# Kernel optimization log

Measured on AMD Instinct MI355X. Metric: run time of the kernel, lower is better.

## Reference

```python
import math
import jax, jax.numpy as jnp
import numpy as np

H = 1024        # hidden_size
V = 32000       # target vocab
T = 64          # decoder steps
B = 32          # batch
NL = 2          # lstm layers
WSZ = 50        # window_size
WLEN = 2 * WSZ + 1
L = 128         # source length (all sequences full)
S = L + WLEN    # padded encoder length, guarantees windows in-bounds
HH = math.ceil(H / 2)
STD2 = (WSZ / 2.0) ** 2
EPS = 1e-14


def setup_inputs():
    key = jax.random.key(0)
    ks = jax.random.split(key, 16)
    sc = 0.02
    inp = {}
    inp["encoder_output"] = jax.random.normal(ks[0], (S, B, H), jnp.float32)
    inp["context"] = jax.random.normal(ks[1], (T, B, H), jnp.float32)
    inp["h0"] = jax.random.normal(ks[2], (NL, B, H), jnp.float32)
    inp["c0"] = jax.random.normal(ks[3], (NL, B, H), jnp.float32)
    inp["embedding"] = jax.random.normal(ks[4], (V, H), jnp.float32) * sc
    inp["attn_w1"] = jax.random.normal(ks[5], (HH, H), jnp.float32) * sc
    inp["attn_b1"] = jnp.zeros((HH,), jnp.float32)
    inp["attn_w2"] = jax.random.normal(ks[6], (1, HH), jnp.float32) * sc
    inp["attn_b2"] = jnp.zeros((1,), jnp.float32)
    inp["lstm_Wih0"] = jax.random.normal(ks[7], (4 * H, 2 * H), jnp.float32) * sc  # input feeding: 2H input
    inp["lstm_Whh0"] = jax.random.normal(ks[8], (4 * H, H), jnp.float32) * sc
    inp["lstm_bih0"] = jnp.zeros((4 * H,), jnp.float32)
    inp["lstm_bhh0"] = jnp.zeros((4 * H,), jnp.float32)
    inp["lstm_Wih1"] = jax.random.normal(ks[9], (4 * H, H), jnp.float32) * sc
    inp["lstm_Whh1"] = jax.random.normal(ks[10], (4 * H, H), jnp.float32) * sc
    inp["lstm_bih1"] = jnp.zeros((4 * H,), jnp.float32)
    inp["lstm_bhh1"] = jnp.zeros((4 * H,), jnp.float32)
    inp["fc1_w"] = jax.random.normal(ks[11], (H, 2 * H), jnp.float32) * sc
    inp["fc1_b"] = jnp.zeros((H,), jnp.float32)
    inp["fc2_w"] = jax.random.normal(ks[12], (V, H), jnp.float32) * sc
    inp["fc2_b"] = jnp.zeros((V,), jnp.float32)
    inp["target_words"] = jax.random.randint(ks[13], (T, B), 0, V)
    inp["lengths"] = jnp.full((B,), L, dtype=jnp.int32)
    return inp


def _lstm_layer(x, h0, c0, Wih, Whh, bih, bhh):
    bias = bih + bhh
    def step(carry, xt):
        h, c = carry
        gates = xt @ Wih.T + h @ Whh.T + bias   # [B, 4H], torch gate order i,f,g,o
        i, f, g, o = jnp.split(gates, 4, axis=-1)
        c = jax.nn.sigmoid(f) * c + jax.nn.sigmoid(i) * jnp.tanh(g)
        h = jax.nn.sigmoid(o) * jnp.tanh(c)
        return (h, c), h
    (hT, cT), ys = jax.lax.scan(step, (h0, c0), x)
    return ys, hT, cT


def _attention(encoder_output, dec_out, lengths, aw1, ab1, aw2, ab2):
    h_s = jnp.transpose(encoder_output, (1, 0, 2))   # [B, S, H]
    h_t = jnp.transpose(dec_out, (1, 0, 2))          # [B, T, H]
    p = jax.nn.sigmoid(jnp.tanh(h_t @ aw1.T + ab1) @ aw2.T + ab2)[..., 0]  # [B, T]
    p = WSZ + lengths[:, None].astype(jnp.float32) * p
    win_start = jnp.round(p - WSZ).astype(jnp.int32)                        # [B, T]
    k = jnp.arange(WLEN)
    positions = win_start[..., None].astype(jnp.float32) + k.astype(jnp.float32)  # [B, T, W]
    gaussian = jnp.exp(-((positions - p[..., None]) ** 2) / (2.0 * STD2))
    # faithful to original: the selection buffer is overwritten every j, so
    # every decoder step attends over the LAST step's window
    sel_idx = win_start[:, -1][:, None] + k                                 # [B, W]
    selection = jnp.take_along_axis(h_s, sel_idx[:, :, None], axis=1)       # [B, W, H]
    score = jnp.einsum('bth,bwh->btw', h_t, selection)
    li = lengths[:, None, None].astype(jnp.int32)
    lo = k[None, None, :] < (WSZ - win_start)[..., None]
    hi = k[None, None, :] >= (li + WSZ - win_start[..., None])
    score = jnp.where(lo | hi, EPS, score)   # original writes epsilon, NOT -inf
    a = jax.nn.softmax(score, axis=2) * gaussian
    c = jnp.einsum('btw,bwh->bth', a, selection)
    return jnp.transpose(c, (1, 0, 2))       # [T, B, H]


def reference(encoder_output, context, h0, c0, embedding,
              attn_w1, attn_b1, attn_w2, attn_b2,
              lstm_Wih0, lstm_Whh0, lstm_bih0, lstm_bhh0,
              lstm_Wih1, lstm_Whh1, lstm_bih1, lstm_bhh1,
              fc1_w, fc1_b, fc2_w, fc2_b,
              target_words, lengths):
    emb = embedding[target_words]                        # [T, B, H]
    x = jnp.concatenate([emb, context], axis=2)          # input feeding -> [T, B, 2H]
    y0, hT0, cT0 = _lstm_layer(x, h0[0], c0[0], lstm_Wih0, lstm_Whh0, lstm_bih0, lstm_bhh0)
    y1, hT1, cT1 = _lstm_layer(y0, h0[1], c0[1], lstm_Wih1, lstm_Whh1, lstm_bih1, lstm_bhh1)
    ctx = _attention(encoder_output, y1, lengths, attn_w1, attn_b1, attn_w2, attn_b2)
    out = jax.nn.relu(jnp.concatenate([ctx, y1], axis=2) @ fc1_w.T + fc1_b)
    y = out @ fc2_w.T + fc2_b                            # [T, B, V]
    h_n = jnp.stack([hT0, hT1])
    c_n = jnp.stack([cT0, cT1])
    return (y, h_n, c_n, ctx)
```

## Files before the change

### kernel.cpp

```cpp
#include <hip/hip_runtime.h>
#include <hip/hip_bf16.h>

#define T_STEPS 64
#define BATCH   32
#define HID     1024
#define VOCAB   32000
#define WLEN_   101
#define WSZ_    50
#define SENC    229
#define LBLK    64

static const size_t Y_SZ   = (size_t)T_STEPS * BATCH * VOCAB;
static const size_t HN_SZ  = (size_t)2 * BATCH * HID;
static const size_t CTX_OFF = Y_SZ + 2 * HN_SZ;

typedef __attribute__((ext_vector_type(8)))  unsigned short us8;
typedef __attribute__((ext_vector_type(8)))  __bf16 bf16x8;
typedef __attribute__((ext_vector_type(4)))  float f32x4;
typedef __attribute__((ext_vector_type(16))) float f32x16;

static __device__ inline unsigned short f2bf(float x) {
    __hip_bfloat16 b = __float2bfloat16(x);
    return __builtin_bit_cast(unsigned short, b);
}

#define GLD_US8_SC(dst, ptr) \
    asm volatile("global_load_dwordx4 %0, %1, off sc0 sc1" : "=v"(dst) : "v"(ptr) : "memory")
#define GLD_F32_SC(dst, ptr) \
    asm volatile("global_load_dword %0, %1, off sc0 sc1" : "=v"(dst) : "v"(ptr) : "memory")
#define GST_U16_SC(ptr, val) \
    asm volatile("global_store_short %0, %1, off sc0 sc1" :: "v"(ptr), "v"(val) : "memory")
#define GST_U32_SC(ptr, val) \
    asm volatile("global_store_dword %0, %1, off sc0 sc1" :: "v"(ptr), "v"(val) : "memory")
#define WAIT_VM0() asm volatile("s_waitcnt vmcnt(0)" ::: "memory")

__global__ __launch_bounds__(256) void gemm_bt(
    const float* __restrict__ A, const float* __restrict__ W,
    const float* __restrict__ b1, const float* __restrict__ b2,
    float* __restrict__ out, int M, int N, int K, int act)
{
    __shared__ __align__(16) float As[16 * 132];
    __shared__ __align__(16) float Ws[16 * 68];
    const int tid  = threadIdx.x;
    const int col0 = blockIdx.x * 64;
    const int row0 = blockIdx.y * 128;
    const int ty   = tid >> 4;
    const int tx   = tid & 15;

    float acc[8][4];
#pragma unroll
    for (int i = 0; i < 8; ++i)
#pragma unroll
        for (int j = 0; j < 4; ++j) acc[i][j] = 0.f;

    for (int k0 = 0; k0 < K; k0 += 16) {
#pragma unroll
        for (int li = 0; li < 2; ++li) {
            int f  = tid + li * 256;
            int r  = f >> 2;
            int kq = (f & 3) << 2;
            float4 v = *reinterpret_cast<const float4*>(A + (size_t)(row0 + r) * K + k0 + kq);
            As[(kq + 0) * 132 + r] = v.x;
            As[(kq + 1) * 132 + r] = v.y;
            As[(kq + 2) * 132 + r] = v.z;
            As[(kq + 3) * 132 + r] = v.w;
        }
        {
            int n  = tid >> 2;
            int kq = (tid & 3) << 2;
            float4 v = *reinterpret_cast<const float4*>(W + (size_t)(col0 + n) * K + k0 + kq);
            Ws[(kq + 0) * 68 + n] = v.x;
            Ws[(kq + 1) * 68 + n] = v.y;
            Ws[(kq + 2) * 68 + n] = v.z;
            Ws[(kq + 3) * 68 + n] = v.w;
        }
        __syncthreads();
#pragma unroll
        for (int k = 0; k < 16; ++k) {
            const float4 a0 = *reinterpret_cast<const float4*>(&As[k * 132 + ty * 8]);
            const float4 a1 = *reinterpret_cast<const float4*>(&As[k * 132 + ty * 8 + 4]);
            const float4 b0 = *reinterpret_cast<const float4*>(&Ws[k * 68 + tx * 4]);
            float av[8] = {a0.x, a0.y, a0.z, a0.w, a1.x, a1.y, a1.z, a1.w};
            float bv[4] = {b0.x, b0.y, b0.z, b0.w};
#pragma unroll
            for (int i = 0; i < 8; ++i)
#pragma unroll
                for (int j = 0; j < 4; ++j) acc[i][j] = fmaf(av[i], bv[j], acc[i][j]);
        }
        __syncthreads();
    }

#pragma unroll
    for (int j = 0; j < 4; ++j) {
        int n = col0 + tx * 4 + j;
        float bias = 0.f;
        if (b1) bias += b1[n];
        if (b2) bias += b2[n];
#pragma unroll
        for (int i = 0; i < 8; ++i) {
            float v = acc[i][j] + bias;
            if (act == 1) v = fmaxf(v, 0.f);
            else if (act == 2) v = tanhf(v);
            out[(size_t)(row0 + ty * 8 + i) * N + n] = v;
        }
    }
}

__global__ __launch_bounds__(256) void gemm_lds_bt(
    const unsigned short* __restrict__ A, const unsigned short* __restrict__ W,
    const float* __restrict__ b1, const float* __restrict__ b2,
    float* __restrict__ out, unsigned short* __restrict__ out_bf,
    int M, int N, int K, int relu, int ntout)
{
    __shared__ __align__(16) unsigned short As[8192];
    __shared__ __align__(16) unsigned short Ws[8192];
    const int tid  = threadIdx.x;
    const int lane = tid & 63;
    const int wave = tid >> 6;

    const int nwg = gridDim.x;
    const int bid = blockIdx.x;
    const int q = nwg >> 3, r8 = nwg & 7;
    const int xcd = bid & 7, sidx = bid >> 3;
    const int wgid = (xcd < r8 ? xcd * (q + 1) : r8 * (q + 1) + (xcd - r8) * q) + sidx;
    const int mt = M >> 7;
    const int row0 = (wgid % mt) << 7;
    const int col0 = (wgid / mt) << 7;

    const int m0   = (wave >> 1) * 64;
    const int n0   = (wave & 1) * 64;
    const int lrow = lane & 15;
    const int kc   = lane >> 4;

    f32x4 acc[4][4];
#pragma unroll
    for (int i = 0; i < 4; ++i)
#pragma unroll
        for (int j = 0; j < 4; ++j) acc[i][j] = (f32x4){0.f, 0.f, 0.f, 0.f};

    const bool isA = (wave < 2);
    const int  lw  = wave & 1;
    const unsigned short* gbase = isA ? (A + (size_t)row0 * K) : (W + (size_t)col0 * K);
    unsigned short* lbase = isA ? As : Ws;

    for (int k0 = 0; k0 < K; k0 += 64) {
#pragma unroll
        for (int i = 0; i < 8; ++i) {
            const int c    = lw * 512 + i * 64 + lane;
            const int row  = c >> 3;
            const int slot = c & 7;
            const unsigned short* src =
                gbase + (size_t)row * K + k0 + ((slot ^ (row & 7)) << 3);
            __builtin_amdgcn_global_load_lds(
                (const __attribute__((address_space(1))) void*)src,
                (__attribute__((address_space(3))) void*)(lbase + (size_t)(lw * 512 + i * 64) * 8),
                16, 0, 0);
        }
        __syncthreads();
#pragma unroll
        for (int ss = 0; ss < 2; ++ss) {
            us8 a[4], b[4];
#pragma unroll
            for (int f = 0; f < 4; ++f) {
                const int ar = m0 + f * 16 + lrow;
                const int as = (ss * 4 + kc) ^ (ar & 7);
                a[f] = *reinterpret_cast<const us8*>(&As[(ar * 8 + as) * 8]);
                const int br = n0 + f * 16 + lrow;
                const int bs = (ss * 4 + kc) ^ (br & 7);
                b[f] = *reinterpret_cast<const us8*>(&Ws[(br * 8 + bs) * 8]);
            }
#pragma unroll
            for (int fi = 0; fi < 4; ++fi)
#pragma unroll
                for (int fj = 0; fj < 4; ++fj)
                    acc[fi][fj] = __builtin_amdgcn_mfma_f32_16x16x32_bf16(
                        __builtin_bit_cast(bf16x8, a[fi]),
                        __builtin_bit_cast(bf16x8, b[fj]),
                        acc[fi][fj], 0, 0, 0);
        }
        __syncthreads();
    }

#pragma unroll
    for (int fi = 0; fi < 4; ++fi)
#pragma unroll
        for (int fj = 0; fj < 4; ++fj) {
            const int cN = col0 + n0 + fj * 16 + lrow;
            float bv = 0.f;
            if (b1) bv += b1[cN];
            if (b2) bv += b2[cN];
#pragma unroll
            for (int j = 0; j < 4; ++j) {
                const int r = row0 + m0 + fi * 16 + (lane >> 4) * 4 + j;
                float v = acc[fi][fj][j] + bv;
                if (relu) v = fmaxf(v, 0.f);
                if (out) {
                    if (ntout) __builtin_nontemporal_store(v, &out[(size_t)r * N + cN]);
                    else       out[(size_t)r * N + cN] = v;
                }
                if (out_bf) out_bf[(size_t)r * N + cN] = f2bf(v);
            }
        }
}

__global__ void prep_kernel(const float* __restrict__ Wih0, unsigned short* __restrict__ Wih0_bf,
                            const float* __restrict__ fc1w, unsigned short* __restrict__ fc1w_bf,
                            const float* __restrict__ emb, const float* __restrict__ ctxin,
                            const int* __restrict__ tw, unsigned short* __restrict__ x_bf,
                            int* __restrict__ flags)
{
    const int bid = blockIdx.x, tid = threadIdx.x;
    if (bid < 2048) {
#pragma unroll
        for (int k = 0; k < 2; ++k) {
            int i = bid * 256 + tid + k * 524288;
            float4 v0 = *reinterpret_cast<const float4*>(Wih0 + (size_t)i * 8);
            float4 v1 = *reinterpret_cast<const float4*>(Wih0 + (size_t)i * 8 + 4);
            us8 c = {f2bf(v0.x), f2bf(v0.y), f2bf(v0.z), f2bf(v0.w),
                     f2bf(v1.x), f2bf(v1.y), f2bf(v1.z), f2bf(v1.w)};
            *reinterpret_cast<us8*>(Wih0_bf + (size_t)i * 8) = c;
        }
    } else if (bid < 3072) {
        int i = (bid - 2048) * 256 + tid;
        float4 v0 = *reinterpret_cast<const float4*>(fc1w + (size_t)i * 8);
        float4 v1 = *reinterpret_cast<const float4*>(fc1w + (size_t)i * 8 + 4);
        us8 c = {f2bf(v0.x), f2bf(v0.y), f2bf(v0.z), f2bf(v0.w),
                 f2bf(v1.x), f2bf(v1.y), f2bf(v1.z), f2bf(v1.w)};
        *reinterpret_cast<us8*>(fc1w_bf + (size_t)i * 8) = c;
    } else if (bid < 3584) {
#pragma unroll
        for (int k = 0; k < 4; ++k) {
            int idx = (bid - 3072) * 256 + tid + k * 131072;
            int row = idx >> 8;
            int c8  = idx & 255;
            const float* src = (c8 < 128)
                ? emb + (size_t)tw[row] * HID + c8 * 8
                : ctxin + (size_t)row * HID + (c8 - 128) * 8;
            float4 v0 = *reinterpret_cast<const float4*>(src);
            float4 v1 = *reinterpret_cast<const float4*>(src + 4);
            us8 c = {f2bf(v0.x), f2bf(v0.y), f2bf(v0.z), f2bf(v0.w),
                     f2bf(v1.x), f2bf(v1.y), f2bf(v1.z), f2bf(v1.w)};
            *reinterpret_cast<us8*>(x_bf + (size_t)idx * 8) = c;
        }
    } else {
        for (int i = tid; i < 6400; i += 256) flags[i] = 0;
    }
}

static __device__ inline void poll_group(int* __restrict__ flags, int gbase, int target)
{
    if (target <= 0) return;
    const int lane = threadIdx.x & 63;
    int* fp = &flags[(gbase + lane) * 32];
    for (;;) {
        int f = __hip_atomic_load(fp, __ATOMIC_RELAXED, __HIP_MEMORY_SCOPE_AGENT);
        if (__all(f >= target)) break;
        __builtin_amdgcn_s_sleep(1);
    }
}

__global__ __launch_bounds__(256) void lstm_fused3(
    const float* __restrict__ gpre0,
    const float* __restrict__ Whh0, const float* __restrict__ Wih1,
    const float* __restrict__ Whh1,
    const float* __restrict__ bih1, const float* __restrict__ bhh1,
    const float* __restrict__ h0all, const float* __restrict__ c0all,
    float* __restrict__ y1o,
    unsigned short* __restrict__ fin_bf,
    float* __restrict__ hn, float* __restrict__ cn,
    unsigned short* __restrict__ hbf,
    float* __restrict__ part,
    int* __restrict__ flags,
    const float* __restrict__ fc2w, unsigned short* __restrict__ fc2w_bf,
    int foldcvt)
{
    __shared__ __align__(16) us8 WB[8192];
    __shared__ float red2[32 * 132];
    __shared__ float csh[512];

    const int tid  = threadIdx.x;
    const int lane = tid & 63;
    const int w    = tid >> 6;
    const int n    = lane & 31;
    const int kh   = lane >> 5;
    const int bid  = blockIdx.x;
    const int role = bid >> 6;
    const int lb   = bid & 63;
    const int j0   = lb * 16;
    const int b    = tid >> 3;
    const int jj   = tid & 7;

    unsigned short* hb0 = hbf;
    unsigned short* hb1 = hbf + 131072;

    {
        const float* Wsrc = (role == 0) ? Whh0 : (role == 1 ? Wih1 : Whh1);
        const int g = n >> 3, cj = n & 7;
#pragma unroll
        for (int T = 0; T < 2; ++T) {
            const float* wrow = Wsrc + (size_t)(g * HID + j0 + T * 8 + cj) * HID;
#pragma unroll
            for (int f = 0; f < 16; ++f) {
                int k = w * 256 + f * 16 + kh * 8;
                float4 v0 = *reinterpret_cast<const float4*>(wrow + k);
                float4 v1 = *reinterpret_cast<const float4*>(wrow + k + 4);
                WB[((T * 4 + w) * 16 + f) * 64 + lane] =
                    (us8){f2bf(v0.x), f2bf(v0.y), f2bf(v0.z), f2bf(v0.w),
                          f2bf(v1.x), f2bf(v1.y), f2bf(v1.z), f2bf(v1.w)};
            }
        }
    }

    float gp[2][4] = {};
    float bb[2][4] = {};
    if (role == 0) {
#pragma unroll
        for (int T = 0; T < 2; ++T) {
            csh[T * 256 + tid] = c0all[b * HID + j0 + T * 8 + jj];
#pragma unroll
            for (int g = 0; g < 4; ++g)
                gp[T][g] = gpre0[(size_t)b * 4096 + g * HID + j0 + T * 8 + jj];
        }
#pragma unroll
        for (int q = 0; q < 2; ++q) {
            int e = lb * 512 + q * 256 + tid;
            unsigned int hv = f2bf(h0all[((e >> 3) & 31) * HID + (e >> 8) * 8 + (e & 7)]);
            GST_U16_SC(hb0 + e, hv);
        }
    } else if (role == 2) {
#pragma unroll
        for (int T = 0; T < 2; ++T) {
            csh[T * 256 + tid] = c0all[32768 + b * HID + j0 + T * 8 + jj];
#pragma unroll
            for (int g = 0; g < 4; ++g)
                bb[T][g] = bih1[g * HID + j0 + T * 8 + jj] + bhh1[g * HID + j0 + T * 8 + jj];
        }
#pragma unroll
        for (int q = 0; q < 2; ++q) {
            int e = lb * 512 + q * 256 + tid;
            unsigned int hv = f2bf(h0all[32768 + ((e >> 3) & 31) * HID + (e >> 8) * 8 + (e & 7)]);
            GST_U16_SC(hb1 + 32768 + e, hv);
        }
    }

    WAIT_VM0();
    __syncthreads();
    if (tid == 0)
        __hip_atomic_store(&flags[bid * 32], 1, __ATOMIC_RELAXED, __HIP_MEMORY_SCOPE_AGENT);

    for (int p = 0; p <= 65; ++p) {
        {
            int g1, t1, g2, t2;
            if (role == 0)      { g1 = 0;   t1 = p + 1; g2 = 64;  t2 = p - 1; }
            else if (role == 1) { g1 = 0;   t1 = p + 1; g2 = 128; t2 = p - 1; }
            else                { g1 = 64;  t1 = p + 1; g2 = 128; t2 = p + 1; }
            if (tid < 64)        poll_group(flags, g1, t1);
            else if (tid < 128)  poll_group(flags, g2, t2);
            __syncthreads();
        }
        const bool active = (role == 0) ? (p <= 63)
                          : (role == 1) ? (p >= 1 && p <= 64)
                                        : (p >= 2);
        if (active) {
            const int t = p - role;
            float pv[2][4];
            if (role == 2) {
                const float* pb = part + (size_t)((p - 2) & 3) * 131072 + lb * 2048 + tid;
#pragma unroll
                for (int T = 0; T < 2; ++T)
#pragma unroll
                    for (int g = 0; g < 4; ++g)
                        GLD_F32_SC(pv[T][g], pb + (T * 4 + g) * 256);
            }
            const unsigned short* hsrc = (role == 2)
                ? hb1 + ((p + 1) & 1) * 32768
                : hb0 + (p & 3) * 32768;
            const unsigned short* hr = hsrc + (size_t)w * 8192 + lane * 8;
            us8 aF[16];
#pragma unroll
            for (int f = 0; f < 16; ++f)
                GLD_US8_SC(aF[f], hr + f * 512);
            WAIT_VM0();
            __builtin_amdgcn_sched_barrier(0);

            f32x16 acc0 = {}, acc1 = {};
#pragma unroll
            for (int f = 0; f < 16; ++f)
                acc0 = __builtin_amdgcn_mfma_f32_32x32x16_bf16(
                    __builtin_bit_cast(bf16x8, aF[f]),
                    __builtin_bit_cast(bf16x8, WB[((0 * 4 + w) * 16 + f) * 64 + lane]),
                    acc0, 0, 0, 0);
#pragma unroll
            for (int f = 0; f < 16; ++f)
                acc1 = __builtin_amdgcn_mfma_f32_32x32x16_bf16(
                    __builtin_bit_cast(bf16x8, aF[f]),
                    __builtin_bit_cast(bf16x8, WB[((1 * 4 + w) * 16 + f) * 64 + lane]),
                    acc1, 0, 0, 0);

#pragma unroll
            for (int T = 0; T < 2; ++T) {
                if (T == 1) __syncthreads();
#pragma unroll
                for (int r = 0; r < 16; ++r) {
                    int m = (r & 3) + 8 * (r >> 2) + 4 * kh;
                    red2[m * 132 + w * 32 + n] = (T == 0) ? acc0[r] : acc1[r];
                }
                __syncthreads();
                float s0, s1, s2, s3;
                {
                    const float* rr = &red2[b * 132 + jj];
                    s0 = rr[0]  + rr[32]  + rr[64]  + rr[96];
                    s1 = rr[8]  + rr[40]  + rr[72]  + rr[104];
                    s2 = rr[16] + rr[48]  + rr[80]  + rr[112];
                    s3 = rr[24] + rr[56]  + rr[88]  + rr[120];
                }
                const int col = j0 + T * 8 + jj;
                const int he  = (lb * 2 + T) * 256 + tid;
                if (role == 1) {
                    float* pdst = part + (size_t)((p - 1) & 3) * 131072 + lb * 2048 + tid;
                    GST_U32_SC(pdst + (T * 4 + 0) * 256, s0);
                    GST_U32_SC(pdst + (T * 4 + 1) * 256, s1);
                    GST_U32_SC(pdst + (T * 4 + 2) * 256, s2);
                    GST_U32_SC(pdst + (T * 4 + 3) * 256, s3);
                } else {
                    if (role == 0) { s0 += gp[T][0]; s1 += gp[T][1]; s2 += gp[T][2]; s3 += gp[T][3]; }
                    else { s0 += pv[T][0] + bb[T][0]; s1 += pv[T][1] + bb[T][1];
                           s2 += pv[T][2] + bb[T][2]; s3 += pv[T][3] + bb[T][3]; }
                    float ig = 1.f / (1.f + expf(-s0));
                    float fg = 1.f / (1.f + expf(-s1));
                    float gg = tanhf(s2);
                    float og = 1.f / (1.f + expf(-s3));
                    float cv = fg * csh[T * 256 + tid] + ig * gg;
                    csh[T * 256 + tid] = cv;
                    float h = og * tanhf(cv);
                    unsigned int hv = f2bf(h);
                    if (role == 0) {
                        GST_U16_SC(hb0 + ((p + 1) & 3) * 32768 + he, hv);
                        if (t == T_STEPS - 1) { hn[b * HID + col] = h; cn[b * HID + col] = cv; }
                    } else {
                        __builtin_nontemporal_store(h, &y1o[(size_t)t * 32768 + b * HID + col]);
                        fin_bf[(size_t)(t * BATCH + b) * 2048 + 1024 + col] = f2bf(h);
                        if (t == T_STEPS - 1) {
                            hn[32768 + b * HID + col] = h;
                            cn[32768 + b * HID + col] = cv;
                        } else {
                            GST_U16_SC(hb1 + (p & 1) * 32768 + he, hv);
                        }
                    }
                }
            }
        }
        if (p < 65) {
            WAIT_VM0();
            __syncthreads();
            if (tid == 0)
                __hip_atomic_store(&flags[bid * 32], p + 2,
                                   __ATOMIC_RELAXED, __HIP_MEMORY_SCOPE_AGENT);
            if (role == 0 && p + 1 <= 63) {
                const float* gsrc = gpre0 + (size_t)((p + 1) * BATCH + b) * 4096 + j0 + jj;
#pragma unroll
                for (int T = 0; T < 2; ++T)
#pragma unroll
                    for (int g = 0; g < 4; ++g)
                        gp[T][g] = gsrc[g * HID + T * 8];
            }
            if (foldcvt && p < 64 && bid >= 64) {
                const int cidx = bid - 64;
                const int base = (p * 128 + cidx) * 500;
                for (int j = tid; j < 500; j += 256) {
                    int i = base + j;
                    if (i < 4096000) {
                        float4 v0 = *reinterpret_cast<const float4*>(fc2w + (size_t)i * 8);
                        float4 v1 = *reinterpret_cast<const float4*>(fc2w + (size_t)i * 8 + 4);
                        us8 c = {f2bf(v0.x), f2bf(v0.y), f2bf(v0.z), f2bf(v0.w),
                                 f2bf(v1.x), f2bf(v1.y), f2bf(v1.z), f2bf(v1.w)};
                        *reinterpret_cast<us8*>(fc2w_bf + (size_t)i * 8) = c;
                    }
                }
            }
        }
    }
}

__global__ __launch_bounds__(64) void attn_p_kernel(
    const float* __restrict__ hidden1, const float* __restrict__ aw2,
    const float* __restrict__ ab2, const int* __restrict__ lengths,
    float* __restrict__ p_arr, int* __restrict__ win_arr)
{
    const int row = blockIdx.x;
    const int lane = threadIdx.x;
    float s = 0.f;
    for (int i = lane; i < 512; i += 64) s += hidden1[(size_t)row * 512 + i] * aw2[i];
    for (int off = 32; off > 0; off >>= 1) s += __shfl_down(s, off);
    if (lane == 0) {
        float v = s + ab2[0];
        float sig = 1.f / (1.f + expf(-v));
        int b = row & 31;
        float lf = (float)lengths[b];
        p_arr[row] = (float)WSZ_ + lf * sig;
        win_arr[row] = (int)rintf(lf * sig);
    }
}

__global__ __launch_bounds__(128) void attn_fused_kernel(
    const float* __restrict__ y1, const float* __restrict__ enc,
    const float* __restrict__ p_arr, const int* __restrict__ win_arr,
    const int* __restrict__ lengths, float* __restrict__ ctx,
    unsigned short* __restrict__ fin_bf)
{
    __shared__ __align__(16) float yl[1024];
    __shared__ float sv[WLEN_];
    __shared__ float av[WLEN_];
    const int row = blockIdx.x;
    const int b   = row & 31;
    const int tid = threadIdx.x;

    for (int i = tid; i < 1024; i += 128) yl[i] = y1[(size_t)row * HID + i];
    __syncthreads();

    const int win = win_arr[row];
    const int wl  = win_arr[(T_STEPS - 1) * BATCH + b];
    const float p = p_arr[row];
    const int len = lengths[b];

    if (tid < WLEN_) {
        const float4* s4 = reinterpret_cast<const float4*>(
            enc + ((size_t)(wl + tid) * BATCH + b) * HID);
        const float4* y4 = reinterpret_cast<const float4*>(yl);
        float acc = 0.f;
        for (int q = 0; q < 256; ++q) {
            float4 a = s4[q]; float4 yy = y4[q];
            acc += a.x * yy.x + a.y * yy.y + a.z * yy.z + a.w * yy.w;
        }
        bool lo = tid < (WSZ_ - win);
        bool hi = tid >= (len + WSZ_ - win);
        sv[tid] = (lo || hi) ? 1e-14f : acc;
    }
    __syncthreads();

    float mx = -1e30f;
    for (int w = 0; w < WLEN_; ++w) mx = fmaxf(mx, sv[w]);
    float sum = 0.f;
    for (int w = 0; w < WLEN_; ++w) sum += expf(sv[w] - mx);
    if (tid < WLEN_) {
        float e = expf(sv[tid] - mx) / sum;
        float d = (float)(win + tid) - p;
        av[tid] = e * expf(-(d * d) / 1250.f);
    }
    __syncthreads();

    float acc[8] = {0, 0, 0, 0, 0, 0, 0, 0};
    for (int w = 0; w < WLEN_; ++w) {
        float a = av[w];
        const float* srow = enc + ((size_t)(wl + w) * BATCH + b) * HID;
#pragma unroll
        for (int i = 0; i < 8; ++i) acc[i] += a * srow[tid + 128 * i];
    }
    for (int i = 0; i < 8; ++i) {
        ctx[(size_t)row * HID + tid + 128 * i] = acc[i];
        fin_bf[(size_t)row * 2048 + tid + 128 * i] = f2bf(acc[i]);
    }
}

__global__ void cvt_bf16_kernel(const float* __restrict__ src,
                                unsigned short* __restrict__ dst, int n8)
{
    for (int i = blockIdx.x * blockDim.x + threadIdx.x; i < n8;
         i += gridDim.x * blockDim.x) {
        float4 v0 = *reinterpret_cast<const float4*>(src + (size_t)i * 8);
        float4 v1 = *reinterpret_cast<const float4*>(src + (size_t)i * 8 + 4);
        us8 c = {f2bf(v0.x), f2bf(v0.y), f2bf(v0.z), f2bf(v0.w),
                 f2bf(v1.x), f2bf(v1.y), f2bf(v1.z), f2bf(v1.w)};
        *reinterpret_cast<us8*>(dst + (size_t)i * 8) = c;
    }
}

extern "C" void kernel_launch(void* const* d_in, const int* in_sizes, int n_in,
                              void* d_out, int out_size, void* d_ws, size_t ws_size,
                              hipStream_t stream)
{
    const float* enc   = (const float*)d_in[0];
    const float* ctxin = (const float*)d_in[1];
    const float* h0    = (const float*)d_in[2];
    const float* c0    = (const float*)d_in[3];
    const float* emb   = (const float*)d_in[4];
    const float* aw1   = (const float*)d_in[5];
    const float* ab1   = (const float*)d_in[6];
    const float* aw2   = (const float*)d_in[7];
    const float* ab2   = (const float*)d_in[8];
    const float* Wih0  = (const float*)d_in[9];
    const float* Whh0  = (const float*)d_in[10];
    const float* bih0  = (const float*)d_in[11];
    const float* bhh0  = (const float*)d_in[12];
    const float* Wih1  = (const float*)d_in[13];
    const float* Whh1  = (const float*)d_in[14];
    const float* bih1  = (const float*)d_in[15];
    const float* bhh1  = (const float*)d_in[16];
    const float* fc1w  = (const float*)d_in[17];
    const float* fc1b  = (const float*)d_in[18];
    const float* fc2w  = (const float*)d_in[19];
    const float* fc2b  = (const float*)d_in[20];
    const int*   tw    = (const int*)d_in[21];
    const int*   lens  = (const int*)d_in[22];

    float* ws = (float*)d_ws;
    float*          buf_gates = ws;
    unsigned short* x_bf      = (unsigned short*)(ws + 8388608);
    float*          buf_part  = ws + 8388608;
    unsigned short* Wih0_bf   = (unsigned short*)(ws + 10485760);
    float*          buf_y1    = ws + 16384000;
    unsigned short* buf_hbf   = (unsigned short*)(ws + 18481152);
    int*            buf_flags = (int*)(ws + 18579456);
    float*          buf_hidden1 = ws + 18587904;
    float*          buf_p     = ws + 19636480;
    int*            buf_win   = (int*)(ws + 19638528);
    unsigned short* fin_bf    = (unsigned short*)(ws + 22917376);
    unsigned short* fc1w_bf   = (unsigned short*)(ws + 25014528);
    unsigned short* fc1out_bf = (unsigned short*)(ws + 26063104);

    const size_t fold_end_bytes = (size_t)(27111680 + 8192000) * 4;
    const int foldcvt = (ws_size >= fold_end_bytes) ? 1 : 0;
    unsigned short* fc2w_bf = foldcvt ? (unsigned short*)(ws + 27111680)
                                      : (unsigned short*)(ws + 8388608);

    if (!foldcvt) fc2w_bf = (unsigned short*)ws;

    float* out   = (float*)d_out;
    float* out_hn  = out + Y_SZ;
    float* out_cn  = out + Y_SZ + HN_SZ;
    float* out_ctx = out + CTX_OFF;

    prep_kernel<<<3585, 256, 0, stream>>>(Wih0, Wih0_bf, fc1w, fc1w_bf,
                                          emb, ctxin, tw, x_bf, buf_flags);

    gemm_lds_bt<<<512, 256, 0, stream>>>(
        x_bf, Wih0_bf, bih0, bhh0, buf_gates, nullptr, 2048, 4096, 2048, 0, 0);

    lstm_fused3<<<3 * LBLK, 256, 0, stream>>>(
        buf_gates, Whh0, Wih1, Whh1, bih1, bhh1, h0, c0,
        buf_y1, fin_bf, out_hn, out_cn, buf_hbf, buf_part,
        buf_flags, fc2w, fc2w_bf, foldcvt);

    if (!foldcvt)
        cvt_bf16_kernel<<<2048, 256, 0, stream>>>(fc2w, fc2w_bf, VOCAB * HID / 8);

    gemm_bt<<<dim3(512 / 64, 2048 / 128), 256, 0, stream>>>(
        buf_y1, aw1, ab1, nullptr, buf_hidden1, 2048, 512, 1024, 2 );
    attn_p_kernel<<<2048, 64, 0, stream>>>(buf_hidden1, aw2, ab2, lens, buf_p, buf_win);
    attn_fused_kernel<<<2048, 128, 0, stream>>>(buf_y1, enc, buf_p, buf_win, lens,
                                                out_ctx, fin_bf);

    gemm_lds_bt<<<128, 256, 0, stream>>>(
        fin_bf, fc1w_bf, fc1b, nullptr, nullptr, fc1out_bf, 2048, 1024, 2048, 1, 0);

    gemm_lds_bt<<<4000, 256, 0, stream>>>(
        fc1out_bf, fc2w_bf, fc2b, nullptr, out, nullptr, 2048, VOCAB, 1024, 0, 1);
}
```

Measured before the change: 938.4 us.

## Fuse attention position kernel into attention and process four timesteps per block

```diff
diff --git a/kernel.cpp b/kernel.cpp
--- a/kernel.cpp
+++ b/kernel.cpp
@@ -482,83 +482,117 @@
     }
 }
 
-__global__ __launch_bounds__(64) void attn_p_kernel(
+__global__ __launch_bounds__(256) void attn_fused4(
+    const float* __restrict__ y1, const float* __restrict__ enc,
     const float* __restrict__ hidden1, const float* __restrict__ aw2,
     const float* __restrict__ ab2, const int* __restrict__ lengths,
-    float* __restrict__ p_arr, int* __restrict__ win_arr)
-{
-    const int row = blockIdx.x;
-    const int lane = threadIdx.x;
-    float s = 0.f;
-    for (int i = lane; i < 512; i += 64) s += hidden1[(size_t)row * 512 + i] * aw2[i];
-    for (int off = 32; off > 0; off >>= 1) s += __shfl_down(s, off);
-    if (lane == 0) {
-        float v = s + ab2[0];
-        float sig = 1.f / (1.f + expf(-v));
-        int b = row & 31;
-        float lf = (float)lengths[b];
-        p_arr[row] = (float)WSZ_ + lf * sig;
-        win_arr[row] = (int)rintf(lf * sig);
-    }
-}
-
-__global__ __launch_bounds__(128) void attn_fused_kernel(
-    const float* __restrict__ y1, const float* __restrict__ enc,
-    const float* __restrict__ p_arr, const int* __restrict__ win_arr,
-    const int* __restrict__ lengths, float* __restrict__ ctx,
-    unsigned short* __restrict__ fin_bf)
-{
-    __shared__ __align__(16) float yl[1024];
-    __shared__ float sv[WLEN_];
-    __shared__ float av[WLEN_];
-    const int row = blockIdx.x;
-    const int b   = row & 31;
-    const int tid = threadIdx.x;
-
-    for (int i = tid; i < 1024; i += 128) yl[i] = y1[(size_t)row * HID + i];
+    float* __restrict__ ctx, unsigned short* __restrict__ fin_bf)
+{
+    __shared__ __align__(16) float yl[4][1024];
+    __shared__ float sv[4][104];
+    __shared__ float av[4][104];
+    __shared__ float p4[4];
+    __shared__ int   win4[4];
+    __shared__ int   winls;
+    const int blk  = blockIdx.x;
+    const int b    = blk >> 4;
+    const int t0   = (blk & 15) * 4;
+    const int tid  = threadIdx.x;
+    const int wv   = tid >> 6;
+    const int lane = tid & 63;
+    const int len  = lengths[b];
+
+    for (int i = tid; i < 4096; i += 256) {
+        int r = i >> 10, h = i & 1023;
+        yl[r][h] = y1[(size_t)((t0 + r) * BATCH + b) * HID + h];
+    }
+
+    {
+        int row = (t0 + wv) * BATCH + b;
+        float s = 0.f;
+        for (int i = lane; i < 512; i += 64) s += hidden1[(size_t)row * 512 + i] * aw2[i];
+        for (int off = 32; off > 0; off >>= 1) s += __shfl_down(s, off);
+        if (lane == 0) {
+            float sig = 1.f / (1.f + expf(-(s + ab2[0])));
+            float lf = (float)len;
+            p4[wv] = (float)WSZ_ + lf * sig;
+            win4[wv] = (int)rintf(lf * sig);
+        }
+        if (wv == 0) {
+            int rowl = (T_STEPS - 1) * BATCH + b;
+            float s2 = 0.f;
+            for (int i = lane; i < 512; i += 64) s2 += hidden1[(size_t)rowl * 512 + i] * aw2[i];
+            for (int off = 32; off > 0; off >>= 1) s2 += __shfl_down(s2, off);
+            if (lane == 0) {
+                float sig = 1.f / (1.f + expf(-(s2 + ab2[0])));
+                winls = (int)rintf((float)len * sig);
+            }
+        }
+    }
     __syncthreads();
-
-    const int win = win_arr[row];
-    const int wl  = win_arr[(T_STEPS - 1) * BATCH + b];
-    const float p = p_arr[row];
-    const int len = lengths[b];
+    const int wl = winls;
 
     if (tid < WLEN_) {
-        const float4* s4 = reinterpret_cast<const float4*>(
+        const float4* s4p = reinterpret_cast<const float4*>(
             enc + ((size_t)(wl + tid) * BATCH + b) * HID);
-        const float4* y4 = reinterpret_cast<const float4*>(yl);
-        float acc = 0.f;
+        const float4* y0 = reinterpret_cast<const float4*>(yl[0]);
+        const float4* y1p = reinterpret_cast<const float4*>(yl[1]);
+        const float4* y2 = reinterpret_cast<const float4*>(yl[2]);
+        const float4* y3 = reinterpret_cast<const float4*>(yl[3]);
+        float a0 = 0.f, a1 = 0.f, a2 = 0.f, a3 = 0.f;
         for (int q = 0; q < 256; ++q) {
-            float4 a = s4[q]; float4 yy = y4[q];
-            acc += a.x * yy.x + a.y * yy.y + a.z * yy.z + a.w * yy.w;
-        }
-        bool lo = tid < (WSZ_ - win);
-        bool hi = tid >= (len + WSZ_ - win);
-        sv[tid] = (lo || hi) ? 1e-14f : acc;
+            float4 a = s4p[q];
+            float4 v0 = y0[q];  a0 += a.x * v0.x + a.y * v0.y + a.z * v0.z + a.w * v0.w;
+            float4 v1 = y1p[q]; a1 += a.x * v1.x + a.y * v1.y + a.z * v1.z + a.w * v1.w;
+            float4 v2 = y2[q];  a2 += a.x * v2.x + a.y * v2.y + a.z * v2.z + a.w * v2.w;
+            float4 v3 = y3[q];  a3 += a.x * v3.x + a.y * v3.y + a.z * v3.z + a.w * v3.w;
+        }
+        float accs[4] = {a0, a1, a2, a3};
+#pragma unroll
+        for (int r = 0; r < 4; ++r) {
+            bool lo = tid < (WSZ_ - win4[r]);
+            bool hi = tid >= (len + WSZ_ - win4[r]);
+            sv[r][tid] = (lo || hi) ? 1e-14f : accs[r];
+        }
     }
     __syncthreads();
 
-    float mx = -1e30f;
-    for (int w = 0; w < WLEN_; ++w) mx = fmaxf(mx, sv[w]);
-    float sum = 0.f;
-    for (int w = 0; w < WLEN_; ++w) sum += expf(sv[w] - mx);
     if (tid < WLEN_) {
-        float e = expf(sv[tid] - mx) / sum;
-        float d = (float)(win + tid) - p;
-        av[tid] = e * expf(-(d * d) / 1250.f);
+#pragma unroll
+        for (int r = 0; r < 4; ++r) {
+            float mx = -1e30f;
+            for (int w = 0; w < WLEN_; ++w) mx = fmaxf(mx, sv[r][w]);
+            float sum = 0.f;
+            for (int w = 0; w < WLEN_; ++w) sum += expf(sv[r][w] - mx);
+            float e = expf(sv[r][tid] - mx) / sum;
+            float d = (float)(win4[r] + tid) - p4[r];
+            av[r][tid] = e * expf(-(d * d) / 1250.f);
+        }
     }
     __syncthreads();
 
-    float acc[8] = {0, 0, 0, 0, 0, 0, 0, 0};
-    for (int w = 0; w < WLEN_; ++w) {
-        float a = av[w];
-        const float* srow = enc + ((size_t)(wl + w) * BATCH + b) * HID;
-#pragma unroll
-        for (int i = 0; i < 8; ++i) acc[i] += a * srow[tid + 128 * i];
-    }
-    for (int i = 0; i < 8; ++i) {
-        ctx[(size_t)row * HID + tid + 128 * i] = acc[i];
-        fin_bf[(size_t)row * 2048 + tid + 128 * i] = f2bf(acc[i]);
+    {
+        const int h0 = tid * 4;
+        float ac[4][4] = {};
+        for (int w = 0; w < WLEN_; ++w) {
+            float4 s = *reinterpret_cast<const float4*>(
+                enc + ((size_t)(wl + w) * BATCH + b) * HID + h0);
+#pragma unroll
+            for (int r = 0; r < 4; ++r) {
+                float a = av[r][w];
+                ac[r][0] += a * s.x; ac[r][1] += a * s.y;
+                ac[r][2] += a * s.z; ac[r][3] += a * s.w;
+            }
+        }
+#pragma unroll
+        for (int r = 0; r < 4; ++r) {
+            size_t row = (size_t)(t0 + r) * BATCH + b;
+#pragma unroll
+            for (int j = 0; j < 4; ++j) {
+                ctx[row * HID + h0 + j] = ac[r][j];
+                fin_bf[row * 2048 + h0 + j] = f2bf(ac[r][j]);
+            }
+        }
     }
 }
 
@@ -612,8 +646,6 @@
     unsigned short* buf_hbf   = (unsigned short*)(ws + 18481152);
     int*            buf_flags = (int*)(ws + 18579456);
     float*          buf_hidden1 = ws + 18587904;
-    float*          buf_p     = ws + 19636480;
-    int*            buf_win   = (int*)(ws + 19638528);
     unsigned short* fin_bf    = (unsigned short*)(ws + 22917376);
     unsigned short* fc1w_bf   = (unsigned short*)(ws + 25014528);
     unsigned short* fc1out_bf = (unsigned short*)(ws + 26063104);
@@ -621,9 +653,7 @@
     const size_t fold_end_bytes = (size_t)(27111680 + 8192000) * 4;
     const int foldcvt = (ws_size >= fold_end_bytes) ? 1 : 0;
     unsigned short* fc2w_bf = foldcvt ? (unsigned short*)(ws + 27111680)
-                                      : (unsigned short*)(ws + 8388608);
-
-    if (!foldcvt) fc2w_bf = (unsigned short*)ws;
+                                      : (unsigned short*)ws;
 
     float* out   = (float*)d_out;
     float* out_hn  = out + Y_SZ;
@@ -646,9 +676,8 @@
 
     gemm_bt<<<dim3(512 / 64, 2048 / 128), 256, 0, stream>>>(
         buf_y1, aw1, ab1, nullptr, buf_hidden1, 2048, 512, 1024, 2 );
-    attn_p_kernel<<<2048, 64, 0, stream>>>(buf_hidden1, aw2, ab2, lens, buf_p, buf_win);
-    attn_fused_kernel<<<2048, 128, 0, stream>>>(buf_y1, enc, buf_p, buf_win, lens,
-                                                out_ctx, fin_bf);
+    attn_fused4<<<512, 256, 0, stream>>>(buf_y1, enc, buf_hidden1, aw2, ab2, lens,
+                                         out_ctx, fin_bf);
 
     gemm_lds_bt<<<128, 256, 0, stream>>>(
         fin_bf, fc1w_bf, fc1b, nullptr, nullptr, fc1out_bf, 2048, 1024, 2048, 1, 0);
```

New measurement: 945.0 us. About the same (+0.7%).
